# Kernel tuning notes

Measured on AMD Instinct MI355X. Metric: run time of the kernel, lower is better.

Reference implementation:

```python
import jax, jax.numpy as jnp
import numpy as np

D_MODEL = 2048
D_INNER = 4096
D_STATE = 16
DT_RANK = 128
D_CONV = 4
EPS = 1e-5


def setup_inputs() -> dict:
    key = jax.random.key(0)
    ks = jax.random.split(key, 10)
    b, l = 1, 1024
    s = 0.02
    x = jax.random.normal(ks[0], (b, l, D_MODEL), jnp.float32)
    w_norm = jnp.ones((D_MODEL,), jnp.float32)
    W_in = jax.random.normal(ks[1], (D_MODEL, 2 * D_INNER), jnp.float32) * s
    conv_w = jax.random.normal(ks[2], (D_CONV, D_INNER), jnp.float32) * 0.3
    conv_b = jnp.zeros((D_INNER,), jnp.float32)
    W_xp = jax.random.normal(ks[3], (D_INNER, DT_RANK + 2 * D_STATE), jnp.float32) * s
    W_dt = jax.random.normal(ks[4], (DT_RANK, D_INNER), jnp.float32) * s
    b_dt = jnp.full((D_INNER,), -4.0, jnp.float32)  # softplus(-4) ~ small dt
    A_log = jnp.log(jnp.tile(jnp.arange(1, D_STATE + 1, dtype=jnp.float32), (D_INNER, 1)))
    D = jnp.ones((D_INNER,), jnp.float32)
    W_out = jax.random.normal(ks[5], (D_INNER, D_MODEL), jnp.float32) * s
    return dict(x=x, w_norm=w_norm, W_in=W_in, conv_w=conv_w, conv_b=conv_b,
                W_xp=W_xp, W_dt=W_dt, b_dt=b_dt, A_log=A_log, D=D, W_out=W_out)


def _rmsnorm(x, w):
    return x * jax.lax.rsqrt(jnp.mean(jnp.square(x), axis=-1, keepdims=True) + EPS) * w


def _depthwise_causal_conv(x, conv_w, conv_b):
    # x: (b, l, d_inner), conv_w: (d_conv, d_inner)
    k = conv_w[:, None, :]  # (W, I/groups=1, O)
    y = jax.lax.conv_general_dilated(
        x, k, window_strides=(1,), padding=((D_CONV - 1, 0),),
        dimension_numbers=('NWC', 'WIO', 'NWC'), feature_group_count=D_INNER)
    return y + conv_b


def _selective_scan(u, delta, A, B, C, D):
    # u, delta: (b,l,d); A: (d,n); B,C: (b,l,n); D: (d,)
    deltaA = jnp.exp(jnp.einsum('bld,dn->bldn', delta, A))          # (b,l,d,n)
    deltaBu = jnp.einsum('bld,bln,bld->bldn', delta, B, u)          # (b,l,d,n)
    dA = jnp.moveaxis(deltaA, 1, 0)    # (l,b,d,n)
    dBu = jnp.moveaxis(deltaBu, 1, 0)  # (l,b,d,n)
    Ct = jnp.moveaxis(C, 1, 0)         # (l,b,n)
    b, l, d = u.shape
    n = A.shape[1]

    def step(h, inputs):
        dA_t, dBu_t, C_t = inputs
        h = h * dA_t + dBu_t                       # (b,d,n)
        y = jnp.einsum('bdn,bn->bd', h, C_t)       # (b,d)
        return h, y

    h0 = jnp.zeros((b, d, n), u.dtype)
    _, ys = jax.lax.scan(step, h0, (dA, dBu, Ct))
    y = jnp.moveaxis(ys, 0, 1)                     # (b,l,d)
    return y + u * D


def reference(x, w_norm, W_in, conv_w, conv_b, W_xp, W_dt, b_dt, A_log, D, W_out):
    # ResidualBlock: out = MambaBlock(RMSNorm(x)) + x
    xn = _rmsnorm(x, w_norm)
    xz = xn @ W_in                                  # (b,l,2*d_inner)
    xs, res = jnp.split(xz, 2, axis=-1)
    xs = _depthwise_causal_conv(xs, conv_w, conv_b)
    xs = jax.nn.silu(xs)
    # SSM
    A = -jnp.exp(A_log)                             # (d_inner, n)
    xdbc = xs @ W_xp                                # (b,l,dt_rank+2n)
    dt_r = xdbc[..., :DT_RANK]
    B = xdbc[..., DT_RANK:DT_RANK + D_STATE]
    C = xdbc[..., DT_RANK + D_STATE:]
    delta = jax.nn.softplus(dt_r @ W_dt + b_dt)     # (b,l,d_inner)
    y = _selective_scan(xs, delta, A, B, C, D)
    y = y * jax.nn.silu(res)
    out = y @ W_out + x
    return out
```

## Files before the change

kernel.cpp:

```cpp
#include <hip/hip_runtime.h>
#include <math.h>

#define L_SEQ   1024
#define DMODEL  2048
#define DINNER  4096
#define DSTATE  16
#define DTRANK  128
#define N_XZ    (2 * DINNER)
#define N_XP    (DTRANK + 2 * DSTATE)
#define EPS_F   1e-5f
#define NCHUNK  32
#define TCH     32
#define SK_XP   16

using bf16x8 = __attribute__((ext_vector_type(8))) short;
using f32x4  = __attribute__((ext_vector_type(4))) float;

__device__ __forceinline__ float silu_f(float v) {
    return v * (1.0f / (1.0f + __expf(-v)));
}
__device__ __forceinline__ float softplus_f(float v) {
    return (v > 15.0f) ? v : log1pf(__expf(v));
}
__device__ __forceinline__ unsigned short f2bf(float f) {
    unsigned b = __float_as_uint(f);
    return (unsigned short)((b + 0x7FFFu + ((b >> 16) & 1u)) >> 16);
}
__device__ __forceinline__ float bf2f(unsigned short u) {
    return __uint_as_float((unsigned)u << 16);
}

#define GLOAD_LDS(gp, lp) \
    __builtin_amdgcn_global_load_lds((const __attribute__((address_space(1))) void*)(gp), \
                                     (__attribute__((address_space(3))) void*)(lp), 16, 0, 0)

__device__ __forceinline__ void transpose_fast(const float* __restrict__ W,
                                               unsigned short* __restrict__ BT,
                                               int K, int N, int bx, int by) {
    const int wave = threadIdx.x >> 6, lane = threadIdx.x & 63;
    const int lr = lane >> 3, lc = lane & 7;
    const int k0 = by * 128 + (wave >> 1) * 64 + lr * 8;
    const int n0 = bx * 128 + (wave & 1) * 64 + lc * 8;
    float v[8][8];
    #pragma unroll
    for (int j = 0; j < 8; ++j) {
        float4 a = *(const float4*)&W[(size_t)(k0 + j) * N + n0];
        float4 b = *(const float4*)&W[(size_t)(k0 + j) * N + n0 + 4];
        v[j][0] = a.x; v[j][1] = a.y; v[j][2] = a.z; v[j][3] = a.w;
        v[j][4] = b.x; v[j][5] = b.y; v[j][6] = b.z; v[j][7] = b.w;
    }
    #pragma unroll
    for (int i = 0; i < 8; ++i) {
        bf16x8 o;
        #pragma unroll
        for (int j = 0; j < 8; ++j) o[j] = (short)f2bf(v[j][i]);
        *(bf16x8*)&BT[(size_t)(n0 + i) * K + k0] = o;
    }
}

__device__ __forceinline__ void transpose_body(const float* __restrict__ W,
                                               unsigned short* __restrict__ BT,
                                               int K, int N, int bx, int by,
                                               unsigned short (*Tl)[72]) {
    const int k0 = by * 64, n0 = bx * 32;
    const int kr = threadIdx.x >> 3;
    const int nc = (threadIdx.x & 7) * 4;
    float4 v0 = *(const float4*)&W[(size_t)(k0 + kr) * N + n0 + nc];
    float4 v1 = *(const float4*)&W[(size_t)(k0 + kr + 32) * N + n0 + nc];
    Tl[nc + 0][kr] = f2bf(v0.x); Tl[nc + 1][kr] = f2bf(v0.y);
    Tl[nc + 2][kr] = f2bf(v0.z); Tl[nc + 3][kr] = f2bf(v0.w);
    Tl[nc + 0][kr + 32] = f2bf(v1.x); Tl[nc + 1][kr + 32] = f2bf(v1.y);
    Tl[nc + 2][kr + 32] = f2bf(v1.z); Tl[nc + 3][kr + 32] = f2bf(v1.w);
    __syncthreads();
    const int n = threadIdx.x >> 3;
    const int k8 = (threadIdx.x & 7) * 8;
    *(bf16x8*)&BT[(size_t)(n0 + n) * K + k0 + k8] = *(const bf16x8*)&Tl[n][k8];
}

__global__ __launch_bounds__(256) void prep_kernel(const float* __restrict__ W_in,
                                                   const float* __restrict__ W_xp,
                                                   const float* __restrict__ W_dt,
                                                   const float* __restrict__ W_out,
                                                   const float* __restrict__ x,
                                                   const float* __restrict__ wn,
                                                   unsigned short* __restrict__ BT_in,
                                                   unsigned short* __restrict__ BTxp,
                                                   unsigned short* __restrict__ BTdt,
                                                   unsigned short* __restrict__ BT_out,
                                                   unsigned short* __restrict__ xn_bf) {
    __shared__ unsigned short Tl[32][72];
    __shared__ float red[4];
    int b = blockIdx.x;
    if (b < 1024) {
        transpose_fast(W_in, BT_in, DMODEL, N_XZ, b & 63, b >> 6);
    } else if (b < 1536) {
        b -= 1024;
        transpose_fast(W_out, BT_out, DINNER, DMODEL, b & 15, b >> 4);
    } else if (b < 1568) {
        b -= 1536;
        transpose_fast(W_dt, BTdt, DTRANK, DINNER, b, 0);
    } else if (b < 1888) {
        b -= 1568;
        transpose_body(W_xp, BTxp, DINNER, N_XP, b % 5, b / 5, Tl);
    } else {
        const int row = b - 1888;
        const float4* xr = (const float4*)(x + (size_t)row * DMODEL);
        float ss = 0.f;
        float4 v0 = xr[threadIdx.x];
        float4 v1 = xr[threadIdx.x + 256];
        ss += v0.x*v0.x + v0.y*v0.y + v0.z*v0.z + v0.w*v0.w;
        ss += v1.x*v1.x + v1.y*v1.y + v1.z*v1.z + v1.w*v1.w;
        #pragma unroll
        for (int o = 32; o > 0; o >>= 1) ss += __shfl_down(ss, o);
        const int lane = threadIdx.x & 63, wv = threadIdx.x >> 6;
        if (lane == 0) red[wv] = ss;
        __syncthreads();
        if (threadIdx.x == 0) {
            float t = red[0] + red[1] + red[2] + red[3];
            red[0] = rsqrtf(t / (float)DMODEL + EPS_F);
        }
        __syncthreads();
        const float scale = red[0];
        const float4* wr = (const float4*)wn;
        float4 w0 = wr[threadIdx.x];
        float4 w1 = wr[threadIdx.x + 256];
        ushort4 o0, o1;
        o0.x = f2bf(v0.x * scale * w0.x); o0.y = f2bf(v0.y * scale * w0.y);
        o0.z = f2bf(v0.z * scale * w0.z); o0.w = f2bf(v0.w * scale * w0.w);
        o1.x = f2bf(v1.x * scale * w1.x); o1.y = f2bf(v1.y * scale * w1.y);
        o1.z = f2bf(v1.z * scale * w1.z); o1.w = f2bf(v1.w * scale * w1.w);
        unsigned short* outr = xn_bf + (size_t)row * DMODEL;
        *(ushort4*)&outr[threadIdx.x * 4] = o0;
        *(ushort4*)&outr[1024 + threadIdx.x * 4] = o1;
    }
}

template <int BM, int BN, int KC, int OUTM>
__global__ __launch_bounds__(256) void gemm_mfma_kernel(const unsigned short* __restrict__ A,
                                                        const unsigned short* __restrict__ BT,
                                                        void* __restrict__ Cv,
                                                        int K, int Kc, int ldc, int Ncols,
                                                        const float* __restrict__ aux) {
    constexpr int MT = BM / 32;
    constexpr int NT = BN / 32;
    __shared__ __align__(16) unsigned short Al[KC * BM * 32];
    __shared__ __align__(16) unsigned short Bl[KC * BN * 32];
    const int tid = threadIdx.x;
    const int lane = tid & 63, wave = tid >> 6;
    const int wm = wave >> 1, wn = wave & 1;
    const int bm = blockIdx.y * BM, bn = blockIdx.x * BN;
    const size_t koff = (size_t)blockIdx.z * Kc;
    float* Cf = (float*)Cv;
    if (OUTM == 2) Cf += (size_t)blockIdx.z * (size_t)gridDim.y * BM * ldc;
    const int sr = lane >> 2;
    const int sk = (((lane & 3) ^ ((sr >> 1) & 3))) * 8;
    const int fr = lane & 15;
    const int fq = lane >> 4;
    const int fsw = (fq ^ ((fr >> 1) & 3)) * 8;

    f32x4 acc[MT][NT];
    #pragma unroll
    for (int i = 0; i < MT; ++i)
        #pragma unroll
        for (int j = 0; j < NT; ++j)
            acc[i][j] = (f32x4){0.f, 0.f, 0.f, 0.f};

    for (int k0 = 0; k0 < Kc; k0 += 32 * KC) {
        #pragma unroll
        for (int p = 0; p < KC; ++p) {
            #pragma unroll
            for (int is = wave; is < BM / 16; is += 4)
                GLOAD_LDS(&A[(size_t)(bm + is * 16 + sr) * K + koff + k0 + p * 32 + sk],
                          &Al[p * BM * 32 + is * 512]);
            #pragma unroll
            for (int is = wave; is < BN / 16; is += 4)
                GLOAD_LDS(&BT[(size_t)(bn + is * 16 + sr) * K + koff + k0 + p * 32 + sk],
                          &Bl[p * BN * 32 + is * 512]);
        }
        __syncthreads();
        #pragma unroll
        for (int p = 0; p < KC; ++p) {
            bf16x8 af[MT], bfr[NT];
            #pragma unroll
            for (int i = 0; i < MT; ++i)
                af[i] = *(const bf16x8*)&Al[p * BM * 32 + (wm * (BM / 2) + i * 16 + fr) * 32 + fsw];
            #pragma unroll
            for (int j = 0; j < NT; ++j)
                bfr[j] = *(const bf16x8*)&Bl[p * BN * 32 + (wn * (BN / 2) + j * 16 + fr) * 32 + fsw];
            #pragma unroll
            for (int i = 0; i < MT; ++i)
                #pragma unroll
                for (int j = 0; j < NT; ++j)
                    acc[i][j] = __builtin_amdgcn_mfma_f32_16x16x32_bf16(af[i], bfr[j], acc[i][j], 0, 0, 0);
        }
        __syncthreads();
    }

    #pragma unroll
    for (int i = 0; i < MT; ++i) {
        const int row = bm + wm * (BM / 2) + i * 16 + fq * 4;
        #pragma unroll
        for (int j = 0; j < NT; ++j) {
            const int col = bn + wn * (BN / 2) + j * 16 + fr;
            if (col < Ncols) {
                #pragma unroll
                for (int r = 0; r < 4; ++r) {
                    float v = acc[i][j][r];
                    if (OUTM == 0) {
                        ((unsigned short*)Cv)[(size_t)(row + r) * ldc + col] = f2bf(v);
                    } else {
                        Cf[(size_t)(row + r) * ldc + col] = v;
                    }
                }
            }
        }
    }
}

__global__ __launch_bounds__(256) void gemm_k128_softplus_kernel(
        const unsigned short* __restrict__ A,
        const unsigned short* __restrict__ BT,
        unsigned short* __restrict__ C,
        const float* __restrict__ bias) {
    const int lane = threadIdx.x & 63, wave = threadIdx.x >> 6;
    const int wm = wave >> 1, wn = wave & 1;
    const int fr = lane & 15, fq = lane >> 4;
    const int bm = blockIdx.y * 64, bn = blockIdx.x * 64;

    bf16x8 af[2][4], bfr[2][4];
    #pragma unroll
    for (int i = 0; i < 2; ++i) {
        const unsigned short* Ap = &A[(size_t)(bm + wm * 32 + i * 16 + fr) * DTRANK + fq * 8];
        #pragma unroll
        for (int kc = 0; kc < 4; ++kc) af[i][kc] = *(const bf16x8*)&Ap[kc * 32];
    }
    #pragma unroll
    for (int j = 0; j < 2; ++j) {
        const unsigned short* Bp = &BT[(size_t)(bn + wn * 32 + j * 16 + fr) * DTRANK + fq * 8];
        #pragma unroll
        for (int kc = 0; kc < 4; ++kc) bfr[j][kc] = *(const bf16x8*)&Bp[kc * 32];
    }

    f32x4 acc[2][2];
    #pragma unroll
    for (int i = 0; i < 2; ++i)
        #pragma unroll
        for (int j = 0; j < 2; ++j)
            acc[i][j] = (f32x4){0.f, 0.f, 0.f, 0.f};
    #pragma unroll
    for (int kc = 0; kc < 4; ++kc)
        #pragma unroll
        for (int i = 0; i < 2; ++i)
            #pragma unroll
            for (int j = 0; j < 2; ++j)
                acc[i][j] = __builtin_amdgcn_mfma_f32_16x16x32_bf16(af[i][kc], bfr[j][kc], acc[i][j], 0, 0, 0);

    #pragma unroll
    for (int i = 0; i < 2; ++i) {
        const int row = bm + wm * 32 + i * 16 + fq * 4;
        #pragma unroll
        for (int j = 0; j < 2; ++j) {
            const int col = bn + wn * 32 + j * 16 + fr;
            const float bc = bias[col];
            #pragma unroll
            for (int r = 0; r < 4; ++r)
                C[(size_t)(row + r) * DINNER + col] = f2bf(softplus_f(acc[i][j][r] + bc));
        }
    }
}

__global__ __launch_bounds__(256) void conv_silu_kernel(const unsigned short* __restrict__ xz_bf,
                                                        const float* __restrict__ cw,
                                                        const float* __restrict__ cb,
                                                        unsigned short* __restrict__ xs_bf) {
    const int idx = blockIdx.x * 256 + threadIdx.x;
    const int t = idx >> 9;
    const int c8 = (idx & 511) * 8;
    float acc[8];
    {
        float4 b0 = *(const float4*)&cb[c8];
        float4 b1 = *(const float4*)&cb[c8 + 4];
        acc[0] = b0.x; acc[1] = b0.y; acc[2] = b0.z; acc[3] = b0.w;
        acc[4] = b1.x; acc[5] = b1.y; acc[6] = b1.z; acc[7] = b1.w;
    }
    #pragma unroll
    for (int k = 0; k < 4; ++k) {
        const int tt = t + k - 3;
        if (tt >= 0) {
            bf16x8 xv = *(const bf16x8*)&xz_bf[(size_t)tt * N_XZ + c8];
            float4 w0 = *(const float4*)&cw[k * DINNER + c8];
            float4 w1 = *(const float4*)&cw[k * DINNER + c8 + 4];
            acc[0] = fmaf(bf2f((unsigned short)xv[0]), w0.x, acc[0]);
            acc[1] = fmaf(bf2f((unsigned short)xv[1]), w0.y, acc[1]);
            acc[2] = fmaf(bf2f((unsigned short)xv[2]), w0.z, acc[2]);
            acc[3] = fmaf(bf2f((unsigned short)xv[3]), w0.w, acc[3]);
            acc[4] = fmaf(bf2f((unsigned short)xv[4]), w1.x, acc[4]);
            acc[5] = fmaf(bf2f((unsigned short)xv[5]), w1.y, acc[5]);
            acc[6] = fmaf(bf2f((unsigned short)xv[6]), w1.z, acc[6]);
            acc[7] = fmaf(bf2f((unsigned short)xv[7]), w1.w, acc[7]);
        }
    }
    bf16x8 o;
    #pragma unroll
    for (int q = 0; q < 8; ++q) o[q] = (short)f2bf(silu_f(acc[q]));
    *(bf16x8*)&xs_bf[(size_t)t * DINNER + c8] = o;
}

__global__ __launch_bounds__(256) void reduce_sk_kernel(const float* __restrict__ part,
                                                        float* __restrict__ xdbc,
                                                        unsigned short* __restrict__ xdbc_dt) {
    const int i = (blockIdx.x * 256 + threadIdx.x) * 4;
    float4 s = make_float4(0.f, 0.f, 0.f, 0.f);
    #pragma unroll
    for (int c = 0; c < SK_XP; ++c) {
        float4 v = *(const float4*)&part[(size_t)c * (L_SEQ * N_XP) + i];
        s.x += v.x; s.y += v.y; s.z += v.z; s.w += v.w;
    }
    *(float4*)&xdbc[i] = s;
    const int col = i % N_XP;
    if (col < DTRANK) {
        ushort4 o;
        o.x = f2bf(s.x); o.y = f2bf(s.y); o.z = f2bf(s.z); o.w = f2bf(s.w);
        *(ushort4*)&xdbc_dt[(i / N_XP) * DTRANK + col] = o;
    }
}

__global__ __launch_bounds__(256) void reduce2_res_kernel(const float* __restrict__ part,
                                                          const float* __restrict__ x,
                                                          float* __restrict__ out) {
    const size_t i = ((size_t)blockIdx.x * 256 + threadIdx.x) * 4;
    float4 a = *(const float4*)&part[i];
    float4 b = *(const float4*)&part[(size_t)L_SEQ * DMODEL + i];
    float4 r = *(const float4*)&x[i];
    float4 o;
    o.x = a.x + b.x + r.x;
    o.y = a.y + b.y + r.y;
    o.z = a.z + b.z + r.z;
    o.w = a.w + b.w + r.w;
    *(float4*)&out[i] = o;
}

__global__ __launch_bounds__(256) void scan_pass1(const unsigned short* __restrict__ delta_bf,
                                                  const unsigned short* __restrict__ xs_bf,
                                                  const float* __restrict__ xdbc,
                                                  const float* __restrict__ A_log,
                                                  float* __restrict__ S,
                                                  float* __restrict__ sumdl) {
    __shared__ float BC[TCH][32];
    const int c = blockIdx.y;
    const int d = blockIdx.x * 256 + threadIdx.x;
    const int t0 = c * TCH;
    {
        const int tt = threadIdx.x >> 3, q = threadIdx.x & 7;
        *(float4*)&BC[tt][q * 4] =
            *(const float4*)&xdbc[(size_t)(t0 + tt) * N_XP + DTRANK + q * 4];
    }
    __syncthreads();
    float Aa[16];
    #pragma unroll
    for (int n = 0; n < 16; ++n) Aa[n] = -__expf(A_log[d * 16 + n]);
    float h[16];
    #pragma unroll
    for (int n = 0; n < 16; ++n) h[n] = 0.f;
    float sd = 0.f;
    for (int t = 0; t < TCH; ++t) {
        const float dl = bf2f(delta_bf[(size_t)(t0 + t) * DINNER + d]);
        const float u  = bf2f(xs_bf[(size_t)(t0 + t) * DINNER + d]);
        sd += dl;
        const float du = dl * u;
        #pragma unroll
        for (int n = 0; n < 16; ++n)
            h[n] = fmaf(h[n], __expf(dl * Aa[n]), du * BC[t][n]);
    }
    float* Sp = &S[((size_t)c * DINNER + d) * 16];
    #pragma unroll
    for (int n = 0; n < 16; n += 4)
        *(float4*)&Sp[n] = make_float4(h[n], h[n + 1], h[n + 2], h[n + 3]);
    sumdl[c * DINNER + d] = sd;
}

__global__ __launch_bounds__(256) void scan_pass2(const float* __restrict__ S,
                                                  const float* __restrict__ sumdl,
                                                  const float* __restrict__ A_log,
                                                  float* __restrict__ h0) {
    const int i = blockIdx.x * 256 + threadIdx.x;
    const int dd = i >> 4;
    const float A = -__expf(A_log[i]);
    float h = 0.f;
    #pragma unroll
    for (int c = 0; c < NCHUNK; ++c) {
        h0[(size_t)c * (DINNER * 16) + i] = h;
        h = h * __expf(A * sumdl[c * DINNER + dd]) + S[(size_t)c * (DINNER * 16) + i];
    }
}

__global__ __launch_bounds__(256) void scan_pass3(const unsigned short* __restrict__ delta_bf,
                                                  const unsigned short* __restrict__ xs_bf,
                                                  const float* __restrict__ xdbc,
                                                  const unsigned short* __restrict__ xz_bf,
                                                  const float* __restrict__ A_log,
                                                  const float* __restrict__ Dp,
                                                  const float* __restrict__ h0,
                                                  unsigned short* __restrict__ yg_bf) {
    __shared__ float BC[TCH][32];
    const int c = blockIdx.y;
    const int d = blockIdx.x * 256 + threadIdx.x;
    const int t0 = c * TCH;
    {
        const int tt = threadIdx.x >> 3, q = threadIdx.x & 7;
        *(float4*)&BC[tt][q * 4] =
            *(const float4*)&xdbc[(size_t)(t0 + tt) * N_XP + DTRANK + q * 4];
    }
    __syncthreads();
    float Aa[16];
    #pragma unroll
    for (int n = 0; n < 16; ++n) Aa[n] = -__expf(A_log[d * 16 + n]);
    float h[16];
    const float* h0p = &h0[(size_t)c * (DINNER * 16) + d * 16];
    #pragma unroll
    for (int n = 0; n < 16; n += 4) {
        float4 v = *(const float4*)&h0p[n];
        h[n] = v.x; h[n + 1] = v.y; h[n + 2] = v.z; h[n + 3] = v.w;
    }
    const float Dd = Dp[d];
    for (int t = 0; t < TCH; ++t) {
        const float dl = bf2f(delta_bf[(size_t)(t0 + t) * DINNER + d]);
        const float u  = bf2f(xs_bf[(size_t)(t0 + t) * DINNER + d]);
        const float du = dl * u;
        float y = 0.f;
        #pragma unroll
        for (int n = 0; n < 16; ++n) {
            h[n] = fmaf(h[n], __expf(dl * Aa[n]), du * BC[t][n]);
            y = fmaf(h[n], BC[t][16 + n], y);
        }
        const float res = bf2f(xz_bf[(size_t)(t0 + t) * N_XZ + DINNER + d]);
        yg_bf[(size_t)(t0 + t) * DINNER + d] = f2bf((y + u * Dd) * silu_f(res));
    }
}

extern "C" void kernel_launch(void* const* d_in, const int* in_sizes, int n_in,
                              void* d_out, int out_size, void* d_ws, size_t ws_size,
                              hipStream_t stream) {
    const float* x     = (const float*)d_in[0];
    const float* wn    = (const float*)d_in[1];
    const float* W_in  = (const float*)d_in[2];
    const float* cw    = (const float*)d_in[3];
    const float* cb    = (const float*)d_in[4];
    const float* W_xp  = (const float*)d_in[5];
    const float* W_dt  = (const float*)d_in[6];
    const float* b_dt  = (const float*)d_in[7];
    const float* A_log = (const float*)d_in[8];
    const float* Dp    = (const float*)d_in[9];
    const float* W_out = (const float*)d_in[10];
    float* out = (float*)d_out;

    float* ws = (float*)d_ws;
    unsigned short* xz_bf    = (unsigned short*)ws;
    unsigned short* xs_bf    = (unsigned short*)(ws + 4194304);
    unsigned short* yg_bf    = (unsigned short*)(ws + 6291456);
    unsigned short* delta_bf = (unsigned short*)(ws + 8388608);
    float*          part     = ws + 10485760;
    float*          S        = ws + 13107200;
    float*          sumdl    = ws + 15204352;
    float*          h0       = ws + 15335424;
    float*          xdbc     = ws + 17432576;
    unsigned short* xn_bf    = (unsigned short*)(ws + 17596416);
    unsigned short* BTxp     = (unsigned short*)(ws + 18644992);
    unsigned short* BTdt     = (unsigned short*)(ws + 18972672);
    unsigned short* xdbc_dt  = (unsigned short*)(ws + 19234816);
    unsigned short* BT_in    = (unsigned short*)(ws + 19300352);
    unsigned short* BT_out   = (unsigned short*)(ws + 27688960);

    prep_kernel<<<2912, 256, 0, stream>>>(W_in, W_xp, W_dt, W_out, x, wn,
                                          BT_in, BTxp, BTdt, BT_out, xn_bf);
    gemm_mfma_kernel<128, 128, 2, 0><<<dim3(N_XZ / 128, L_SEQ / 128), 256, 0, stream>>>(
        xn_bf, BT_in, xz_bf, DMODEL, DMODEL, N_XZ, N_XZ, nullptr);
    conv_silu_kernel<<<(L_SEQ * DINNER / 8) / 256, 256, 0, stream>>>(xz_bf, cw, cb, xs_bf);
    gemm_mfma_kernel<64, 64, 2, 2><<<dim3(3, L_SEQ / 64, SK_XP), 256, 0, stream>>>(
        xs_bf, BTxp, part, DINNER, DINNER / SK_XP, N_XP, N_XP, nullptr);
    reduce_sk_kernel<<<(L_SEQ * N_XP / 4) / 256, 256, 0, stream>>>(part, xdbc, xdbc_dt);
    gemm_k128_softplus_kernel<<<dim3(DINNER / 64, L_SEQ / 64), 256, 0, stream>>>(
        xdbc_dt, BTdt, delta_bf, b_dt);
    scan_pass1<<<dim3(DINNER / 256, NCHUNK), 256, 0, stream>>>(delta_bf, xs_bf, xdbc, A_log, S, sumdl);
    scan_pass2<<<(DINNER * 16) / 256, 256, 0, stream>>>(S, sumdl, A_log, h0);
    scan_pass3<<<dim3(DINNER / 256, NCHUNK), 256, 0, stream>>>(delta_bf, xs_bf, xdbc, xz_bf,
                                                               A_log, Dp, h0, yg_bf);
    gemm_mfma_kernel<64, 128, 2, 2><<<dim3(DMODEL / 128, L_SEQ / 64, 2), 256, 0, stream>>>(
        yg_bf, BT_out, part, DINNER, DINNER / 2, DMODEL, DMODEL, nullptr);
    reduce2_res_kernel<<<(L_SEQ * DMODEL) / 1024, 256, 0, stream>>>(part, x, out);
}
```

Baseline: 334.7 us.

## Pre-pack weights into MFMA tile blocks and fuse the residual into the out-projection GEMM

The prep kernel now writes W_in and W_out as bf16 in 16x32 tile-blocked order, so each B-operand global-to-LDS load in the GEMM reads one contiguous 1 KB block instead of 16 strided rows. The out-projection split-K is done as two back-to-back GEMM launches: the first writes the partial sum plus the residual x, and the second accumulates into the output. This removes the reduce2 kernel and the partial-buffer round trip. The cost is a serial dependency between the two half-K launches, each with half the previous grid, which may reduce occupancy. The prep kernel also gets more, smaller transpose blocks.

```diff
diff --git a/kernel.cpp b/kernel.cpp
--- a/kernel.cpp
+++ b/kernel.cpp
@@ -33,6 +33,37 @@
 #define GLOAD_LDS(gp, lp) \
     __builtin_amdgcn_global_load_lds((const __attribute__((address_space(1))) void*)(gp), \
                                      (__attribute__((address_space(3))) void*)(lp), 16, 0, 0)
+
+__device__ __forceinline__ void transpose_blocked(const float* __restrict__ W,
+                                                  unsigned short* __restrict__ BTb,
+                                                  int K, int N, int bx, int by,
+                                                  unsigned short* Tb) {
+    const int tid = threadIdx.x;
+    const int n0 = bx * 64, k0 = by * 128;
+    #pragma unroll
+    for (int i = 0; i < 8; ++i) {
+        const int r = i * 16 + (tid >> 4);
+        const int c = (tid & 15) * 4;
+        float4 v = *(const float4*)&W[(size_t)(k0 + r) * N + n0 + c];
+        Tb[(c + 0) * 136 + r] = f2bf(v.x);
+        Tb[(c + 1) * 136 + r] = f2bf(v.y);
+        Tb[(c + 2) * 136 + r] = f2bf(v.z);
+        Tb[(c + 3) * 136 + r] = f2bf(v.w);
+    }
+    __syncthreads();
+    const int wave = tid >> 6, lane = tid & 63;
+    const int kblocks = K >> 5;
+    #pragma unroll
+    for (int t = 0; t < 4; ++t) {
+        const int ob = wave * 4 + t;
+        const int nb = ob >> 2, kb = ob & 3;
+        const int n = nb * 16 + (lane >> 2);
+        const int k = kb * 32 + (lane & 3) * 8;
+        bf16x8 v = *(const bf16x8*)&Tb[n * 136 + k];
+        const size_t blk = (size_t)(((n0 >> 4) + nb)) * kblocks + ((k0 >> 5) + kb);
+        *(bf16x8*)&BTb[blk * 512 + (size_t)lane * 8] = v;
+    }
+}
 
 __device__ __forceinline__ void transpose_fast(const float* __restrict__ W,
                                                unsigned short* __restrict__ BT,
@@ -88,22 +119,23 @@
                                                    unsigned short* __restrict__ BTdt,
                                                    unsigned short* __restrict__ BT_out,
                                                    unsigned short* __restrict__ xn_bf) {
+    __shared__ __align__(16) unsigned short Tb[64 * 136];
     __shared__ unsigned short Tl[32][72];
     __shared__ float red[4];
     int b = blockIdx.x;
-    if (b < 1024) {
-        transpose_fast(W_in, BT_in, DMODEL, N_XZ, b & 63, b >> 6);
-    } else if (b < 1536) {
-        b -= 1024;
-        transpose_fast(W_out, BT_out, DINNER, DMODEL, b & 15, b >> 4);
-    } else if (b < 1568) {
-        b -= 1536;
+    if (b < 2048) {
+        transpose_blocked(W_in, BT_in, DMODEL, N_XZ, b & 127, b >> 7, Tb);
+    } else if (b < 3072) {
+        b -= 2048;
+        transpose_blocked(W_out, BT_out, DINNER, DMODEL, b & 31, b >> 5, Tb);
+    } else if (b < 3104) {
+        b -= 3072;
         transpose_fast(W_dt, BTdt, DTRANK, DINNER, b, 0);
-    } else if (b < 1888) {
-        b -= 1568;
+    } else if (b < 3424) {
+        b -= 3104;
         transpose_body(W_xp, BTxp, DINNER, N_XP, b % 5, b / 5, Tl);
     } else {
-        const int row = b - 1888;
+        const int row = b - 3424;
         const float4* xr = (const float4*)(x + (size_t)row * DMODEL);
         float ss = 0.f;
         float4 v0 = xr[threadIdx.x];
@@ -135,7 +167,7 @@
     }
 }
 
-template <int BM, int BN, int KC, int OUTM>
+template <int BM, int BN, int KC, int OUTM, int BLK>
 __global__ __launch_bounds__(256) void gemm_mfma_kernel(const unsigned short* __restrict__ A,
                                                         const unsigned short* __restrict__ BT,
                                                         void* __restrict__ Cv,
@@ -173,9 +205,17 @@
                 GLOAD_LDS(&A[(size_t)(bm + is * 16 + sr) * K + koff + k0 + p * 32 + sk],
                           &Al[p * BM * 32 + is * 512]);
             #pragma unroll
-            for (int is = wave; is < BN / 16; is += 4)
-                GLOAD_LDS(&BT[(size_t)(bn + is * 16 + sr) * K + koff + k0 + p * 32 + sk],
-                          &Bl[p * BN * 32 + is * 512]);
+            for (int is = wave; is < BN / 16; is += 4) {
+                if (BLK) {
+                    const size_t blk = (size_t)((bn >> 4) + is) * (K >> 5)
+                                     + ((koff + k0 + p * 32) >> 5);
+                    GLOAD_LDS(&BT[blk * 512 + sr * 32 + sk],
+                              &Bl[p * BN * 32 + is * 512]);
+                } else {
+                    GLOAD_LDS(&BT[(size_t)(bn + is * 16 + sr) * K + koff + k0 + p * 32 + sk],
+                              &Bl[p * BN * 32 + is * 512]);
+                }
+            }
         }
         __syncthreads();
         #pragma unroll
@@ -208,8 +248,13 @@
                     float v = acc[i][j][r];
                     if (OUTM == 0) {
                         ((unsigned short*)Cv)[(size_t)(row + r) * ldc + col] = f2bf(v);
+                    } else if (OUTM == 2) {
+                        Cf[(size_t)(row + r) * ldc + col] = v;
+                    } else if (OUTM == 3) {
+                        Cf[(size_t)(row + r) * ldc + col] =
+                            v + aux[(size_t)(row + r) * ldc + col];
                     } else {
-                        Cf[(size_t)(row + r) * ldc + col] = v;
+                        Cf[(size_t)(row + r) * ldc + col] += v;
                     }
                 }
             }
@@ -323,21 +368,6 @@
         o.x = f2bf(s.x); o.y = f2bf(s.y); o.z = f2bf(s.z); o.w = f2bf(s.w);
         *(ushort4*)&xdbc_dt[(i / N_XP) * DTRANK + col] = o;
     }
-}
-
-__global__ __launch_bounds__(256) void reduce2_res_kernel(const float* __restrict__ part,
-                                                          const float* __restrict__ x,
-                                                          float* __restrict__ out) {
-    const size_t i = ((size_t)blockIdx.x * 256 + threadIdx.x) * 4;
-    float4 a = *(const float4*)&part[i];
-    float4 b = *(const float4*)&part[(size_t)L_SEQ * DMODEL + i];
-    float4 r = *(const float4*)&x[i];
-    float4 o;
-    o.x = a.x + b.x + r.x;
-    o.y = a.y + b.y + r.y;
-    o.z = a.z + b.z + r.z;
-    o.w = a.w + b.w + r.w;
-    *(float4*)&out[i] = o;
 }
 
 __global__ __launch_bounds__(256) void scan_pass1(const unsigned short* __restrict__ delta_bf,
@@ -471,12 +501,12 @@
     unsigned short* BT_in    = (unsigned short*)(ws + 19300352);
     unsigned short* BT_out   = (unsigned short*)(ws + 27688960);
 
-    prep_kernel<<<2912, 256, 0, stream>>>(W_in, W_xp, W_dt, W_out, x, wn,
+    prep_kernel<<<4448, 256, 0, stream>>>(W_in, W_xp, W_dt, W_out, x, wn,
                                           BT_in, BTxp, BTdt, BT_out, xn_bf);
-    gemm_mfma_kernel<128, 128, 2, 0><<<dim3(N_XZ / 128, L_SEQ / 128), 256, 0, stream>>>(
+    gemm_mfma_kernel<128, 128, 2, 0, 1><<<dim3(N_XZ / 128, L_SEQ / 128), 256, 0, stream>>>(
         xn_bf, BT_in, xz_bf, DMODEL, DMODEL, N_XZ, N_XZ, nullptr);
     conv_silu_kernel<<<(L_SEQ * DINNER / 8) / 256, 256, 0, stream>>>(xz_bf, cw, cb, xs_bf);
-    gemm_mfma_kernel<64, 64, 2, 2><<<dim3(3, L_SEQ / 64, SK_XP), 256, 0, stream>>>(
+    gemm_mfma_kernel<64, 64, 2, 2, 0><<<dim3(3, L_SEQ / 64, SK_XP), 256, 0, stream>>>(
         xs_bf, BTxp, part, DINNER, DINNER / SK_XP, N_XP, N_XP, nullptr);
     reduce_sk_kernel<<<(L_SEQ * N_XP / 4) / 256, 256, 0, stream>>>(part, xdbc, xdbc_dt);
     gemm_k128_softplus_kernel<<<dim3(DINNER / 64, L_SEQ / 64), 256, 0, stream>>>(
@@ -485,7 +515,8 @@
     scan_pass2<<<(DINNER * 16) / 256, 256, 0, stream>>>(S, sumdl, A_log, h0);
     scan_pass3<<<dim3(DINNER / 256, NCHUNK), 256, 0, stream>>>(delta_bf, xs_bf, xdbc, xz_bf,
                                                                A_log, Dp, h0, yg_bf);
-    gemm_mfma_kernel<64, 128, 2, 2><<<dim3(DMODEL / 128, L_SEQ / 64, 2), 256, 0, stream>>>(
-        yg_bf, BT_out, part, DINNER, DINNER / 2, DMODEL, DMODEL, nullptr);
-    reduce2_res_kernel<<<(L_SEQ * DMODEL) / 1024, 256, 0, stream>>>(part, x, out);
-}
+    gemm_mfma_kernel<64, 128, 2, 3, 1><<<dim3(DMODEL / 128, L_SEQ / 64), 256, 0, stream>>>(
+        yg_bf, BT_out, out, DINNER, DINNER / 2, DMODEL, DMODEL, x);
+    gemm_mfma_kernel<64, 128, 2, 4, 1><<<dim3(DMODEL / 128, L_SEQ / 64), 256, 0, stream>>>(
+        yg_bf + 2048, BT_out + 64 * 512, out, DINNER, DINNER / 2, DMODEL, DMODEL, nullptr);
+}
```

After: 352.0 us. 5.2% more time.

## Store transposed bf16 weights in 16x32 blocked tiles for contiguous GEMM loads

Applied to the files above, without the earlier changes.

The W_in and W_out transposes now write bf16 weights in a blocked layout of 16-row by 32-k tiles, each 512 elements and contiguous. The two big GEMMs index B through this layout, so each wave's LDS fill reads one contiguous 1 KB chunk instead of 16 strided rows. Each transpose block also handles 256 columns instead of 128, halving the prep grid. The cost is more registers per thread in the transpose and scattered 16-byte stores when writing the blocked layout.

```diff
diff --git a/kernel.cpp b/kernel.cpp
--- a/kernel.cpp
+++ b/kernel.cpp
@@ -33,6 +33,41 @@
 #define GLOAD_LDS(gp, lp) \
     __builtin_amdgcn_global_load_lds((const __attribute__((address_space(1))) void*)(gp), \
                                      (__attribute__((address_space(3))) void*)(lp), 16, 0, 0)
+
+__device__ __forceinline__ void transpose_fast2b(const float* __restrict__ W,
+                                                 unsigned short* __restrict__ BTb,
+                                                 int K, int N, int bx, int by) {
+    const int wave = threadIdx.x >> 6, lane = threadIdx.x & 63;
+    const int lr = lane >> 3, lc = lane & 7;
+    const int k0 = by * 128 + (wave >> 1) * 64 + lr * 8;
+    const int nb = bx * 256 + (wave & 1) * 128;
+    const int kblocks = K >> 5;
+    float v[2][8][8];
+    #pragma unroll
+    for (int j = 0; j < 8; ++j) {
+        #pragma unroll
+        for (int p = 0; p < 2; ++p) {
+            const float* rp = &W[(size_t)(k0 + j) * N + nb + p * 64 + lc * 8];
+            float4 a = *(const float4*)rp;
+            float4 b = *(const float4*)(rp + 4);
+            v[p][j][0] = a.x; v[p][j][1] = a.y; v[p][j][2] = a.z; v[p][j][3] = a.w;
+            v[p][j][4] = b.x; v[p][j][5] = b.y; v[p][j][6] = b.z; v[p][j][7] = b.w;
+        }
+    }
+    #pragma unroll
+    for (int p = 0; p < 2; ++p) {
+        const int n0 = nb + p * 64 + lc * 8;
+        #pragma unroll
+        for (int i = 0; i < 8; ++i) {
+            bf16x8 o;
+            #pragma unroll
+            for (int j = 0; j < 8; ++j) o[j] = (short)f2bf(v[p][j][i]);
+            const int gn = n0 + i;
+            const size_t blk = (size_t)(gn >> 4) * kblocks + (k0 >> 5);
+            *(bf16x8*)&BTb[blk * 512 + (gn & 15) * 32 + (k0 & 31)] = o;
+        }
+    }
+}
 
 __device__ __forceinline__ void transpose_fast(const float* __restrict__ W,
                                                unsigned short* __restrict__ BT,
@@ -91,19 +126,19 @@
     __shared__ unsigned short Tl[32][72];
     __shared__ float red[4];
     int b = blockIdx.x;
-    if (b < 1024) {
-        transpose_fast(W_in, BT_in, DMODEL, N_XZ, b & 63, b >> 6);
-    } else if (b < 1536) {
-        b -= 1024;
-        transpose_fast(W_out, BT_out, DINNER, DMODEL, b & 15, b >> 4);
-    } else if (b < 1568) {
-        b -= 1536;
+    if (b < 512) {
+        transpose_fast2b(W_in, BT_in, DMODEL, N_XZ, b & 31, b >> 5);
+    } else if (b < 768) {
+        b -= 512;
+        transpose_fast2b(W_out, BT_out, DINNER, DMODEL, b & 7, b >> 3);
+    } else if (b < 800) {
+        b -= 768;
         transpose_fast(W_dt, BTdt, DTRANK, DINNER, b, 0);
-    } else if (b < 1888) {
-        b -= 1568;
+    } else if (b < 1120) {
+        b -= 800;
         transpose_body(W_xp, BTxp, DINNER, N_XP, b % 5, b / 5, Tl);
     } else {
-        const int row = b - 1888;
+        const int row = b - 1120;
         const float4* xr = (const float4*)(x + (size_t)row * DMODEL);
         float ss = 0.f;
         float4 v0 = xr[threadIdx.x];
@@ -135,7 +170,7 @@
     }
 }
 
-template <int BM, int BN, int KC, int OUTM>
+template <int BM, int BN, int KC, int OUTM, int BLK>
 __global__ __launch_bounds__(256) void gemm_mfma_kernel(const unsigned short* __restrict__ A,
                                                         const unsigned short* __restrict__ BT,
                                                         void* __restrict__ Cv,
@@ -173,9 +208,17 @@
                 GLOAD_LDS(&A[(size_t)(bm + is * 16 + sr) * K + koff + k0 + p * 32 + sk],
                           &Al[p * BM * 32 + is * 512]);
             #pragma unroll
-            for (int is = wave; is < BN / 16; is += 4)
-                GLOAD_LDS(&BT[(size_t)(bn + is * 16 + sr) * K + koff + k0 + p * 32 + sk],
-                          &Bl[p * BN * 32 + is * 512]);
+            for (int is = wave; is < BN / 16; is += 4) {
+                if (BLK) {
+                    const size_t blk = (size_t)((bn >> 4) + is) * (K >> 5)
+                                     + ((koff + k0 + p * 32) >> 5);
+                    GLOAD_LDS(&BT[blk * 512 + sr * 32 + sk],
+                              &Bl[p * BN * 32 + is * 512]);
+                } else {
+                    GLOAD_LDS(&BT[(size_t)(bn + is * 16 + sr) * K + koff + k0 + p * 32 + sk],
+                              &Bl[p * BN * 32 + is * 512]);
+                }
+            }
         }
         __syncthreads();
         #pragma unroll
@@ -471,12 +514,12 @@
     unsigned short* BT_in    = (unsigned short*)(ws + 19300352);
     unsigned short* BT_out   = (unsigned short*)(ws + 27688960);
 
-    prep_kernel<<<2912, 256, 0, stream>>>(W_in, W_xp, W_dt, W_out, x, wn,
+    prep_kernel<<<2144, 256, 0, stream>>>(W_in, W_xp, W_dt, W_out, x, wn,
                                           BT_in, BTxp, BTdt, BT_out, xn_bf);
-    gemm_mfma_kernel<128, 128, 2, 0><<<dim3(N_XZ / 128, L_SEQ / 128), 256, 0, stream>>>(
+    gemm_mfma_kernel<128, 128, 2, 0, 1><<<dim3(N_XZ / 128, L_SEQ / 128), 256, 0, stream>>>(
         xn_bf, BT_in, xz_bf, DMODEL, DMODEL, N_XZ, N_XZ, nullptr);
     conv_silu_kernel<<<(L_SEQ * DINNER / 8) / 256, 256, 0, stream>>>(xz_bf, cw, cb, xs_bf);
-    gemm_mfma_kernel<64, 64, 2, 2><<<dim3(3, L_SEQ / 64, SK_XP), 256, 0, stream>>>(
+    gemm_mfma_kernel<64, 64, 2, 2, 0><<<dim3(3, L_SEQ / 64, SK_XP), 256, 0, stream>>>(
         xs_bf, BTxp, part, DINNER, DINNER / SK_XP, N_XP, N_XP, nullptr);
     reduce_sk_kernel<<<(L_SEQ * N_XP / 4) / 256, 256, 0, stream>>>(part, xdbc, xdbc_dt);
     gemm_k128_softplus_kernel<<<dim3(DINNER / 64, L_SEQ / 64), 256, 0, stream>>>(
@@ -485,7 +528,7 @@
     scan_pass2<<<(DINNER * 16) / 256, 256, 0, stream>>>(S, sumdl, A_log, h0);
     scan_pass3<<<dim3(DINNER / 256, NCHUNK), 256, 0, stream>>>(delta_bf, xs_bf, xdbc, xz_bf,
                                                                A_log, Dp, h0, yg_bf);
-    gemm_mfma_kernel<64, 128, 2, 2><<<dim3(DMODEL / 128, L_SEQ / 64, 2), 256, 0, stream>>>(
+    gemm_mfma_kernel<64, 128, 2, 2, 1><<<dim3(DMODEL / 128, L_SEQ / 64, 2), 256, 0, stream>>>(
         yg_bf, BT_out, part, DINNER, DINNER / 2, DMODEL, DMODEL, nullptr);
     reduce2_res_kernel<<<(L_SEQ * DMODEL) / 1024, 256, 0, stream>>>(part, x, out);
 }
```

After: 340.0 us. About the same (+1.6%).
